# Kernel optimization log

Hardware: AMD Instinct MI355X
Metric: run time of the kernel (lower is better)

Reference implementation:

```python
import jax, jax.numpy as jnp
import numpy as np

EMBED_DIM = 1024
ATTN_DIM = 1024


def setup_inputs() -> dict:
    key = jax.random.key(0)
    k1, k2, k3, k4 = jax.random.split(key, 4)
    embedded = jax.random.normal(k1, (4, 2048, EMBED_DIM), dtype=jnp.float32)
    # torch nn.Linear weights are [out_features, in_features]
    s = 1.0 / np.sqrt(EMBED_DIM)
    Wk = jax.random.uniform(k2, (ATTN_DIM, EMBED_DIM), jnp.float32, -s, s)
    Wq = jax.random.uniform(k3, (ATTN_DIM, EMBED_DIM), jnp.float32, -s, s)
    Wv = jax.random.uniform(k4, (ATTN_DIM, EMBED_DIM), jnp.float32, -s, s)
    return {"embedded": embedded, "Wk": Wk, "Wq": Wq, "Wv": Wv}


def reference(embedded, Wk, Wq, Wv):
    # projections: x @ W.T  (torch Linear, no bias)
    k = jnp.einsum("bse,ae->bsa", embedded, Wk)
    q = jnp.einsum("bse,ae->bsa", embedded, Wq)
    v = jnp.einsum("bse,ae->bsa", embedded, Wv)
    scale = 1.0 / jnp.sqrt(jnp.float32(ATTN_DIM))
    attn = jnp.einsum("bqa,bka->bqk", q, k) * scale  # [B, S, S]
    S = attn.shape[1]
    causal = jnp.tril(jnp.ones((S, S), dtype=bool))
    attn = jnp.where(causal[None, :, :], attn, -jnp.inf)
    a = jax.nn.softmax(attn, axis=2)
    out = jnp.einsum("bqk,bka->bqa", a, v)
    return jnp.round(out, 4)
```

## Files before the change

### kernel.cpp

```cpp
#include <hip/hip_runtime.h>
#include <hip/hip_bf16.h>
#include <hip/hip_fp16.h>
#include <stdint.h>

typedef __bf16 bf16_t;
typedef bf16_t bf16x8 __attribute__((ext_vector_type(8)));
typedef bf16_t bf16x4 __attribute__((ext_vector_type(4)));
typedef _Float16 f16x8 __attribute__((ext_vector_type(8)));
typedef float f32x4 __attribute__((ext_vector_type(4)));

#define BM 128
#define BN 128
#define BK 32

__device__ __forceinline__ void gload_lds16(const void* g, void* l) {
    __builtin_amdgcn_global_load_lds(
        (const __attribute__((address_space(1))) void*)(uintptr_t)g,
        (__attribute__((address_space(3))) void*)(uintptr_t)l,
        16, 0, 0);
}

template <int EPI>
__device__ __forceinline__ void gemm_body(
    bf16_t* __restrict__ As, bf16_t* __restrict__ Bs,
    const bf16_t* __restrict__ A, long lda,
    const bf16_t* __restrict__ B, long ldb,
    void* __restrict__ Cv, long ldc,
    int k0beg, int k1end, float scale, int m0, int n0)
{
    const int tid = threadIdx.x;
    const int wid = tid >> 6, lane = tid & 63;
    const int wr = wid >> 1, wc = wid & 1;
    const int hw = lane >> 4, ln = lane & 15;

    const bf16_t *srcA[2], *srcB[2];
#pragma unroll
    for (int i = 0; i < 2; i++) {
        const int c = tid + i * 256;
        const int row = c >> 2;
        const int j = ((c & 3) - (row >> 1)) & 3;
        srcA[i] = A + (size_t)(m0 + row) * lda + j * 8;
        srcB[i] = B + (size_t)(n0 + row) * ldb + j * 8;
    }

    f32x4 acc[4][4] = {};

    for (int k0 = k0beg; k0 < k1end; k0 += BK) {
        gload_lds16(srcA[0] + k0, &As[wid * 512]);
        gload_lds16(srcA[1] + k0, &As[2048 + wid * 512]);
        gload_lds16(srcB[0] + k0, &Bs[wid * 512]);
        gload_lds16(srcB[1] + k0, &Bs[2048 + wid * 512]);
        __syncthreads();

        bf16x8 af[4], bfr[4];
#pragma unroll
        for (int t = 0; t < 4; t++) {
            const int r  = wr * 64 + t * 16 + ln;
            const int rb = wc * 64 + t * 16 + ln;
            af[t]  = *(const bf16x8*)&As[r  * BK + (((hw + (r  >> 1)) & 3) * 8)];
            bfr[t] = *(const bf16x8*)&Bs[rb * BK + (((hw + (rb >> 1)) & 3) * 8)];
        }
#pragma unroll
        for (int ti = 0; ti < 4; ti++)
#pragma unroll
            for (int tj = 0; tj < 4; tj++)
                acc[ti][tj] = __builtin_amdgcn_mfma_f32_16x16x32_bf16(
                    af[ti], bfr[tj], acc[ti][tj], 0, 0, 0);
        __syncthreads();
    }

#pragma unroll
    for (int ti = 0; ti < 4; ti++) {
        const int rbase = m0 + wr * 64 + ti * 16 + hw * 4;
#pragma unroll
        for (int tj = 0; tj < 4; tj++) {
            const int col = n0 + wc * 64 + tj * 16 + ln;
            if (EPI == 4) {
                const int bb = rbase >> 11;
                const int s  = rbase & 2047;
                const int d  = col - 2048;
                bf16x4 o;
#pragma unroll
                for (int rg = 0; rg < 4; rg++) o[rg] = (bf16_t)acc[ti][tj][rg];
                *(bf16x4*)&((bf16_t*)Cv)[(size_t)bb * 2097152 + (size_t)d * 2048 + s] = o;
            } else {
#pragma unroll
                for (int rg = 0; rg < 4; rg++) {
                    const float v = acc[ti][tj][rg] * scale;
                    const size_t idx = (size_t)(rbase + rg) * ldc + col;
                    if (EPI == 0)      ((bf16_t*)Cv)[idx]   = (bf16_t)v;
                    else if (EPI == 1) ((_Float16*)Cv)[idx] = (_Float16)v;
                    else               ((float*)Cv)[idx]    = v;
                }
            }
        }
    }
}

__global__ __launch_bounds__(256) void gemm1_qkv(
    const bf16_t* __restrict__ xb, const bf16_t* __restrict__ Wb,
    bf16_t* __restrict__ QKVb, bf16_t* __restrict__ Vt)
{
    __shared__ __align__(16) bf16_t As[BM * BK];
    __shared__ __align__(16) bf16_t Bs[BN * BK];
    const int lin = blockIdx.x;
    const int xcd = lin & 7;
    const int j   = lin >> 3;
    const int p   = j >> 6;
    const int w   = j & 63;
    const int mblk = xcd * 8 + (w >> 3);
    const int nblk = p * 8 + (w & 7);
    const int m0 = mblk * BM, n0 = nblk * BN;
    if (nblk < 16)
        gemm_body<0>(As, Bs, xb, 1024, Wb, 1024, QKVb, 2048, 0, 1024, 1.0f, m0, n0);
    else
        gemm_body<4>(As, Bs, xb, 1024, Wb, 1024, Vt, 2048, 0, 1024, 1.0f, m0, n0);
}

__global__ __launch_bounds__(256) void qk_gemm(
    const bf16_t* __restrict__ QKVb, _Float16* __restrict__ S)
{
    __shared__ __align__(16) bf16_t As[BM * BK];
    __shared__ __align__(16) bf16_t Bs[BN * BK];
    const int b = blockIdx.x & 3;
    int rem = blockIdx.x >> 2;
    int my = 15, nx = 0;
#pragma unroll
    for (int m = 15; m >= 0; --m) {
        if (rem < m + 1) { my = m; nx = rem; break; }
        rem -= m + 1;
    }
    const bf16_t* base = QKVb + (size_t)b * (2048L * 2048);
    gemm_body<1>(As, Bs,
                 base + 1024, 2048,
                 base, 2048,
                 S + (size_t)b * (2048L * 2048), 2048,
                 0, 1024, 0.03125f, my * BM, nx * BN);
}

__global__ __launch_bounds__(256) void gemm3_pv(
    const bf16_t* __restrict__ P, const bf16_t* __restrict__ Vt,
    float* __restrict__ out)
{
    __shared__ __align__(16) bf16_t As[BM * BK];
    __shared__ __align__(16) bf16_t Bs[BN * BK];
    const int id = blockIdx.x;
    const int strip = 15 - (id >> 5);
    const int nx = (id >> 2) & 7;
    const int b = id & 3;
    const int m0 = strip * BM;
    gemm_body<2>(As, Bs,
                 P + (size_t)b * (2048L * 2048), 2048,
                 Vt + (size_t)b * (1024L * 2048), 2048,
                 out + (size_t)b * (2048L * 1024), 1024,
                 0, m0 + BM, 1.0f, m0, nx * BN);
}

__global__ __launch_bounds__(256) void cast_all(
    const float* __restrict__ x,
    const float* __restrict__ Wk, const float* __restrict__ Wq,
    const float* __restrict__ Wv,
    bf16_t* __restrict__ xb, bf16_t* __restrict__ Wb)
{
    const int blk = blockIdx.x;
    const float* src;
    bf16_t* dst;
    if (blk < 8192) {
        const size_t i = ((size_t)blk * 256 + threadIdx.x) * 4;
        src = x + i;
        dst = xb + i;
    } else {
        const size_t j = ((size_t)(blk - 8192) * 256 + threadIdx.x) * 4;
        dst = Wb + j;
        if (j < (size_t)1048576)      src = Wk + j;
        else if (j < (size_t)2097152) src = Wq + (j - 1048576);
        else                          src = Wv + (j - 2097152);
    }
    const float4 v = *(const float4*)src;
    bf16x4 o;
    o.x = (bf16_t)v.x; o.y = (bf16_t)v.y; o.z = (bf16_t)v.z; o.w = (bf16_t)v.w;
    *(bf16x4*)dst = o;
}

__device__ __forceinline__ float wred_max(float v) {
#pragma unroll
    for (int o = 32; o; o >>= 1) v = fmaxf(v, __shfl_xor(v, o, 64));
    return v;
}
__device__ __forceinline__ float wred_sum(float v) {
#pragma unroll
    for (int o = 32; o; o >>= 1) v += __shfl_xor(v, o, 64);
    return v;
}

__global__ __launch_bounds__(256) void softmax_rows(_Float16* __restrict__ S)
{
    __shared__ float red[8];
    const int r = blockIdx.x;
    const int i = r & 2047;
    const int n = i + 1;
    _Float16* row = S + (size_t)r * 2048;
    const int tid = threadIdx.x;
    const int wid = tid >> 6, lane = tid & 63;
    const int base = tid * 8;

    const f16x8 v8 = *(const f16x8*)(row + base);
    float vals[8];
    float mx = -3e30f;
#pragma unroll
    for (int k = 0; k < 8; k++) {
        const float v = (base + k < n) ? (float)v8[k] : -3e30f;
        vals[k] = v;
        mx = fmaxf(mx, v);
    }
    mx = wred_max(mx);
    if (lane == 0) red[wid] = mx;
    __syncthreads();
    mx = fmaxf(fmaxf(red[0], red[1]), fmaxf(red[2], red[3]));

    float s = 0.f;
#pragma unroll
    for (int k = 0; k < 8; k++) {
        const float e = __expf(vals[k] - mx);
        vals[k] = e;
        s += e;
    }
    s = wred_sum(s);
    if (lane == 0) red[4 + wid] = s;
    __syncthreads();
    s = red[4] + red[5] + red[6] + red[7];
    const float inv = 1.0f / s;

    bf16x8 o;
#pragma unroll
    for (int k = 0; k < 8; k++) o[k] = (bf16_t)(vals[k] * inv);
    *(bf16x8*)((bf16_t*)row + base) = o;
}

extern "C" void kernel_launch(void* const* d_in, const int* in_sizes, int n_in,
                              void* d_out, int out_size, void* d_ws, size_t ws_size,
                              hipStream_t stream)
{
    const float* x  = (const float*)d_in[0];
    const float* Wk = (const float*)d_in[1];
    const float* Wq = (const float*)d_in[2];
    const float* Wv = (const float*)d_in[3];
    char* ws = (char*)d_ws;

    bf16_t*   QKVb = (bf16_t*)(ws);
    bf16_t*   Vt   = (bf16_t*)(ws + ((size_t)32 << 20));
    bf16_t*   xb   = (bf16_t*)(ws + ((size_t)48 << 20));
    bf16_t*   Wb   = (bf16_t*)(ws + ((size_t)64 << 20));
    _Float16* S    = (_Float16*)(ws + ((size_t)48 << 20));
    float*    out  = (float*)d_out;

    cast_all<<<11264, 256, 0, stream>>>(x, Wk, Wq, Wv, xb, Wb);

    gemm1_qkv<<<1536, 256, 0, stream>>>(xb, Wb, QKVb, Vt);

    qk_gemm<<<544, 256, 0, stream>>>(QKVb, S);

    softmax_rows<<<8192, 256, 0, stream>>>(S);

    gemm3_pv<<<512, 256, 0, stream>>>((bf16_t*)S, Vt, out);
}
```

Baseline: 238.3 us.

## Fuse softmax into QK epilogue with atomic rowsums and deferred normalization

Removes the separate softmax kernel: the QK GEMM epilogue applies the causal mask, computes exp of scaled scores directly to bf16, and accumulates per-row sums via shuffle reductions and atomics. The PV GEMM divides its output rows by the stored sums. This eliminates a full read/write pass over the score matrix and one launch, at the cost of dropping max subtraction, which can overflow for large-magnitude scores, and of atomic traffic.

```diff
diff --git a/kernel.cpp b/kernel.cpp
--- a/kernel.cpp
+++ b/kernel.cpp
@@ -6,7 +6,6 @@
 typedef __bf16 bf16_t;
 typedef bf16_t bf16x8 __attribute__((ext_vector_type(8)));
 typedef bf16_t bf16x4 __attribute__((ext_vector_type(4)));
-typedef _Float16 f16x8 __attribute__((ext_vector_type(8)));
 typedef float f32x4 __attribute__((ext_vector_type(4)));
 
 #define BM 128
@@ -26,7 +25,8 @@
     const bf16_t* __restrict__ A, long lda,
     const bf16_t* __restrict__ B, long ldb,
     void* __restrict__ Cv, long ldc,
-    int k0beg, int k1end, float scale, int m0, int n0)
+    int k0beg, int k1end, float scale, int m0, int n0,
+    float* __restrict__ rs)
 {
     const int tid = threadIdx.x;
     const int wid = tid >> 6, lane = tid & 63;
@@ -72,6 +72,13 @@
 #pragma unroll
     for (int ti = 0; ti < 4; ti++) {
         const int rbase = m0 + wr * 64 + ti * 16 + hw * 4;
+        f32x4 inv4;
+        if (EPI == 2) {
+            const float4 r4 = *(const float4*)&rs[rbase];
+            inv4[0] = 1.0f / r4.x; inv4[1] = 1.0f / r4.y;
+            inv4[2] = 1.0f / r4.z; inv4[3] = 1.0f / r4.w;
+        }
+        float part[4] = {0.f, 0.f, 0.f, 0.f};
 #pragma unroll
         for (int tj = 0; tj < 4; tj++) {
             const int col = n0 + wc * 64 + tj * 16 + ln;
@@ -86,12 +93,29 @@
             } else {
 #pragma unroll
                 for (int rg = 0; rg < 4; rg++) {
-                    const float v = acc[ti][tj][rg] * scale;
                     const size_t idx = (size_t)(rbase + rg) * ldc + col;
-                    if (EPI == 0)      ((bf16_t*)Cv)[idx]   = (bf16_t)v;
-                    else if (EPI == 1) ((_Float16*)Cv)[idx] = (_Float16)v;
-                    else               ((float*)Cv)[idx]    = v;
+                    if (EPI == 0) {
+                        ((bf16_t*)Cv)[idx] = (bf16_t)(acc[ti][tj][rg]);
+                    } else if (EPI == 2) {
+                        ((float*)Cv)[idx] = acc[ti][tj][rg] * inv4[rg];
+                    } else {
+                        const float e = (col <= rbase + rg)
+                                      ? __expf(acc[ti][tj][rg] * scale) : 0.0f;
+                        part[rg] += e;
+                        ((bf16_t*)Cv)[idx] = (bf16_t)e;
+                    }
                 }
+            }
+        }
+        if (EPI == 3) {
+#pragma unroll
+            for (int rg = 0; rg < 4; rg++) {
+                float p = part[rg];
+                p += __shfl_xor(p, 1, 64);
+                p += __shfl_xor(p, 2, 64);
+                p += __shfl_xor(p, 4, 64);
+                p += __shfl_xor(p, 8, 64);
+                if (ln == 0) atomicAdd(&rs[rbase + rg], p);
             }
         }
     }
@@ -112,13 +136,16 @@
     const int nblk = p * 8 + (w & 7);
     const int m0 = mblk * BM, n0 = nblk * BN;
     if (nblk < 16)
-        gemm_body<0>(As, Bs, xb, 1024, Wb, 1024, QKVb, 2048, 0, 1024, 1.0f, m0, n0);
+        gemm_body<0>(As, Bs, xb, 1024, Wb, 1024, QKVb, 2048,
+                     0, 1024, 1.0f, m0, n0, nullptr);
     else
-        gemm_body<4>(As, Bs, xb, 1024, Wb, 1024, Vt, 2048, 0, 1024, 1.0f, m0, n0);
+        gemm_body<4>(As, Bs, xb, 1024, Wb, 1024, Vt, 2048,
+                     0, 1024, 1.0f, m0, n0, nullptr);
 }
 
 __global__ __launch_bounds__(256) void qk_gemm(
-    const bf16_t* __restrict__ QKVb, _Float16* __restrict__ S)
+    const bf16_t* __restrict__ QKVb, bf16_t* __restrict__ E,
+    float* __restrict__ rowsum)
 {
     __shared__ __align__(16) bf16_t As[BM * BK];
     __shared__ __align__(16) bf16_t Bs[BN * BK];
@@ -131,16 +158,17 @@
         rem -= m + 1;
     }
     const bf16_t* base = QKVb + (size_t)b * (2048L * 2048);
-    gemm_body<1>(As, Bs,
+    gemm_body<3>(As, Bs,
                  base + 1024, 2048,
                  base, 2048,
-                 S + (size_t)b * (2048L * 2048), 2048,
-                 0, 1024, 0.03125f, my * BM, nx * BN);
+                 E + (size_t)b * (2048L * 2048), 2048,
+                 0, 1024, 0.03125f, my * BM, nx * BN,
+                 rowsum + b * 2048);
 }
 
 __global__ __launch_bounds__(256) void gemm3_pv(
-    const bf16_t* __restrict__ P, const bf16_t* __restrict__ Vt,
-    float* __restrict__ out)
+    const bf16_t* __restrict__ E, const bf16_t* __restrict__ Vt,
+    const float* __restrict__ rowsum, float* __restrict__ out)
 {
     __shared__ __align__(16) bf16_t As[BM * BK];
     __shared__ __align__(16) bf16_t Bs[BN * BK];
@@ -150,19 +178,26 @@
     const int b = id & 3;
     const int m0 = strip * BM;
     gemm_body<2>(As, Bs,
-                 P + (size_t)b * (2048L * 2048), 2048,
+                 E + (size_t)b * (2048L * 2048), 2048,
                  Vt + (size_t)b * (1024L * 2048), 2048,
                  out + (size_t)b * (2048L * 1024), 1024,
-                 0, m0 + BM, 1.0f, m0, nx * BN);
+                 0, m0 + BM, 1.0f, m0, nx * BN,
+                 (float*)rowsum + b * 2048);
 }
 
 __global__ __launch_bounds__(256) void cast_all(
     const float* __restrict__ x,
     const float* __restrict__ Wk, const float* __restrict__ Wq,
     const float* __restrict__ Wv,
-    bf16_t* __restrict__ xb, bf16_t* __restrict__ Wb)
+    bf16_t* __restrict__ xb, bf16_t* __restrict__ Wb,
+    float* __restrict__ rowsum)
 {
     const int blk = blockIdx.x;
+    if (blk >= 11264) {
+        const size_t i = ((size_t)(blk - 11264) * 256 + threadIdx.x) * 4;
+        *(float4*)(rowsum + i) = make_float4(0.f, 0.f, 0.f, 0.f);
+        return;
+    }
     const float* src;
     bf16_t* dst;
     if (blk < 8192) {
@@ -182,61 +217,6 @@
     *(bf16x4*)dst = o;
 }
 
-__device__ __forceinline__ float wred_max(float v) {
-#pragma unroll
-    for (int o = 32; o; o >>= 1) v = fmaxf(v, __shfl_xor(v, o, 64));
-    return v;
-}
-__device__ __forceinline__ float wred_sum(float v) {
-#pragma unroll
-    for (int o = 32; o; o >>= 1) v += __shfl_xor(v, o, 64);
-    return v;
-}
-
-__global__ __launch_bounds__(256) void softmax_rows(_Float16* __restrict__ S)
-{
-    __shared__ float red[8];
-    const int r = blockIdx.x;
-    const int i = r & 2047;
-    const int n = i + 1;
-    _Float16* row = S + (size_t)r * 2048;
-    const int tid = threadIdx.x;
-    const int wid = tid >> 6, lane = tid & 63;
-    const int base = tid * 8;
-
-    const f16x8 v8 = *(const f16x8*)(row + base);
-    float vals[8];
-    float mx = -3e30f;
-#pragma unroll
-    for (int k = 0; k < 8; k++) {
-        const float v = (base + k < n) ? (float)v8[k] : -3e30f;
-        vals[k] = v;
-        mx = fmaxf(mx, v);
-    }
-    mx = wred_max(mx);
-    if (lane == 0) red[wid] = mx;
-    __syncthreads();
-    mx = fmaxf(fmaxf(red[0], red[1]), fmaxf(red[2], red[3]));
-
-    float s = 0.f;
-#pragma unroll
-    for (int k = 0; k < 8; k++) {
-        const float e = __expf(vals[k] - mx);
-        vals[k] = e;
-        s += e;
-    }
-    s = wred_sum(s);
-    if (lane == 0) red[4 + wid] = s;
-    __syncthreads();
-    s = red[4] + red[5] + red[6] + red[7];
-    const float inv = 1.0f / s;
-
-    bf16x8 o;
-#pragma unroll
-    for (int k = 0; k < 8; k++) o[k] = (bf16_t)(vals[k] * inv);
-    *(bf16x8*)((bf16_t*)row + base) = o;
-}
-
 extern "C" void kernel_launch(void* const* d_in, const int* in_sizes, int n_in,
                               void* d_out, int out_size, void* d_ws, size_t ws_size,
                               hipStream_t stream)
@@ -247,20 +227,19 @@
     const float* Wv = (const float*)d_in[3];
     char* ws = (char*)d_ws;
 
-    bf16_t*   QKVb = (bf16_t*)(ws);
-    bf16_t*   Vt   = (bf16_t*)(ws + ((size_t)32 << 20));
-    bf16_t*   xb   = (bf16_t*)(ws + ((size_t)48 << 20));
-    bf16_t*   Wb   = (bf16_t*)(ws + ((size_t)64 << 20));
-    _Float16* S    = (_Float16*)(ws + ((size_t)48 << 20));
-    float*    out  = (float*)d_out;
-
-    cast_all<<<11264, 256, 0, stream>>>(x, Wk, Wq, Wv, xb, Wb);
+    bf16_t* QKVb   = (bf16_t*)(ws);
+    bf16_t* Vt     = (bf16_t*)(ws + ((size_t)32 << 20));
+    bf16_t* xb     = (bf16_t*)(ws + ((size_t)48 << 20));
+    bf16_t* Wb     = (bf16_t*)(ws + ((size_t)64 << 20));
+    bf16_t* E      = (bf16_t*)(ws + ((size_t)48 << 20));
+    float*  rowsum = (float*)(ws + ((size_t)80 << 20));
+    float*  out    = (float*)d_out;
+
+    cast_all<<<11272, 256, 0, stream>>>(x, Wk, Wq, Wv, xb, Wb, rowsum);
 
     gemm1_qkv<<<1536, 256, 0, stream>>>(xb, Wb, QKVb, Vt);
 
-    qk_gemm<<<544, 256, 0, stream>>>(QKVb, S);
-
-    softmax_rows<<<8192, 256, 0, stream>>>(S);
-
-    gemm3_pv<<<512, 256, 0, stream>>>((bf16_t*)S, Vt, out);
-}
+    qk_gemm<<<544, 256, 0, stream>>>(QKVb, E, rowsum);
+
+    gemm3_pv<<<512, 256, 0, stream>>>(E, Vt, rowsum, out);
+}
```

Result: faster. 226.2 us (-5.1%).
